# Kernel tuning notes

Measured on AMD Instinct MI355X. Metric: run time of the kernel, lower is better.

The kernel has to match this reference:

```python
import jax, jax.numpy as jnp
import numpy as np

B, N, C, KV = 4, 4096, 1024, 1024
H = 4            # hardcoded 4-way split in the source
Ch, Kh = C // H, KV // H
EPS = 1e-5       # InstanceNorm2d default eps


def setup_inputs() -> dict:
    key = jax.random.key(0)
    ks = jax.random.split(key, 12)
    s = 0.02
    return {
        "emb1":     jax.random.normal(ks[0], (B, N, C),  jnp.float32),
        "emb_all":  jax.random.normal(ks[1], (B, N, KV), jnp.float32),
        "embd1":    jax.random.normal(ks[2], (B, N, C),  jnp.float32),
        "emb_alld": jax.random.normal(ks[3], (B, N, KV), jnp.float32),
        # per-head query weights (distinct per split), torch Linear layout [out,in]
        "Wq":   jax.random.normal(ks[4],  (H, Ch, Ch), jnp.float32) * s,
        "Wqd":  jax.random.normal(ks[5],  (H, Ch, Ch), jnp.float32) * s,
        # source reuses key[0]/value[0] for all splits -> single shared weight
        "Wk0":  jax.random.normal(ks[6],  (Kh, Kh), jnp.float32) * s,
        "Wv0":  jax.random.normal(ks[7],  (Kh, Kh), jnp.float32) * s,
        "Wkd0": jax.random.normal(ks[8],  (Kh, Kh), jnp.float32) * s,
        "Wvd0": jax.random.normal(ks[9],  (Kh, Kh), jnp.float32) * s,
        "Wout":  jax.random.normal(ks[10], (C, C), jnp.float32) * s,
        "Woutd": jax.random.normal(ks[11], (C, C), jnp.float32) * s,
    }


def _inorm(s):
    # InstanceNorm2d(affine=False): normalize over the (C/4, KV/4) plane per (b, head)
    m = s.mean(axis=(2, 3), keepdims=True)
    v = ((s - m) ** 2).mean(axis=(2, 3), keepdims=True)
    return (s - m) * jax.lax.rsqrt(v + EPS)


def reference(emb1, emb_all, embd1, emb_alld,
              Wq, Wqd, Wk0, Wv0, Wkd0, Wvd0, Wout, Woutd):
    scale = 1.0 / np.sqrt(KV).astype(np.float32)
    # split into 4 channel groups and project (Q: per-group weight; K/V: shared weight)
    Q  = jnp.einsum('bnhc,hoc->bhno', emb1.reshape(B, N, H, Ch),  Wq)    # [B,H,N,Ch]
    Qd = jnp.einsum('bnhc,hoc->bhno', embd1.reshape(B, N, H, Ch), Wqd)
    K  = jnp.einsum('bnhk,ok->bhno', emb_all.reshape(B, N, H, Kh),  Wk0)  # [B,H,N,Kh]
    V  = jnp.einsum('bnhk,ok->bhno', emb_all.reshape(B, N, H, Kh),  Wv0)
    Kd = jnp.einsum('bnhk,ok->bhno', emb_alld.reshape(B, N, H, Kh), Wkd0)
    Vd = jnp.einsum('bnhk,ok->bhno', emb_alld.reshape(B, N, H, Kh), Wvd0)
    # channel-attention scores: contract over tokens N -> [B,H,Ch,Kh]
    s1  = jnp.einsum('bhnc,bhnk->bhck', Q,  Kd) * scale
    sd1 = jnp.einsum('bhnc,bhnk->bhck', Qd, K)  * scale
    p1  = jax.nn.softmax(_inorm(s1),  axis=-1)
    pd1 = jax.nn.softmax(_inorm(sd1), axis=-1)
    # context: probs @ V^T -> [b,h,c,n]; permute(0,3,2,1)+view -> [B,N,C] (c-major, h-minor)
    ctx1  = jnp.einsum('bhck,bhnk->bnch', p1,  Vd).reshape(B, N, C)
    ctxd1 = jnp.einsum('bhck,bhnk->bnch', pd1, V ).reshape(B, N, C)
    O1  = ctx1  @ Wout.T
    Od1 = ctxd1 @ Woutd.T
    return (O1, Od1)
```

## Files before the change

kernel.cpp:

```cpp
#include <hip/hip_runtime.h>
#include <math.h>


#define PITCH 40

typedef __bf16 bf16x4 __attribute__((ext_vector_type(4)));
typedef __bf16 bf16x8 __attribute__((ext_vector_type(8)));
typedef float f32x4 __attribute__((ext_vector_type(4)));

__device__ inline void gl2lds16(const void* g, void* l) {
    __builtin_amdgcn_global_load_lds(
        (const __attribute__((address_space(1))) unsigned int*)g,
        (__attribute__((address_space(3))) unsigned int*)l, 16, 0, 0);
}

__global__ __launch_bounds__(256) void prep_x(const float* __restrict__ emb_all,
                                              const float* __restrict__ emb_alld,
                                              __bf16* __restrict__ Xb) {
    const float* src = blockIdx.y ? emb_alld : emb_all;
    __bf16* dst = Xb + (long long)blockIdx.y * 16777216;
    long long i4 = (long long)blockIdx.x * 256 + threadIdx.x;
    float4 v = *(const float4*)&src[i4 * 4];
    bf16x4 o = {(__bf16)v.x, (__bf16)v.y, (__bf16)v.z, (__bf16)v.w};
    *(bf16x4*)&dst[i4 * 4] = o;
}

__global__ __launch_bounds__(256) void prep_w(
    const float* __restrict__ Wq, const float* __restrict__ Wqd,
    const float* __restrict__ Wk0, const float* __restrict__ Wv0,
    const float* __restrict__ Wkd0, const float* __restrict__ Wvd0,
    const float* __restrict__ Wout, const float* __restrict__ Woutd,
    __bf16* __restrict__ Wq_bf, __bf16* __restrict__ Wk_bf,
    __bf16* __restrict__ WvT_bf, __bf16* __restrict__ WoutR_bf)
{
    int id = blockIdx.x * 256 + threadIdx.x;
    if (id < 524288) {
        Wq_bf[id] = (__bf16)(id < 262144 ? Wq[id] : Wqd[id - 262144]);
    } else if (id < 655360) {
        int j = id - 524288;
        Wk_bf[j] = (__bf16)(j < 65536 ? Wkd0[j] : Wk0[j - 65536]);
    } else if (id < 786432) {
        int j = id - 655360;
        int p = j >> 16, r = (j >> 8) & 255, c2 = j & 255;
        const float* s = p ? Wv0 : Wvd0;
        WvT_bf[j] = (__bf16)s[c2 * 256 + r];
    } else if (id < 2883584) {
        int j = id - 786432;
        int p = j >> 20; int rem = j & 1048575; int h = rem >> 18; int oc = rem & 262143;
        int o = oc >> 8, c = oc & 255;
        const float* s = p ? Woutd : Wout;
        WoutR_bf[j] = (__bf16)s[o * 1024 + c * 4 + h];
    }
}

__global__ __launch_bounds__(256) void gram_mfma(
    const float* __restrict__ emb1, const float* __restrict__ emb_all,
    const float* __restrict__ embd1, const float* __restrict__ emb_alld,
    float* __restrict__ Gpart)
{
    __shared__ __bf16 As[128 * PITCH];
    __shared__ __bf16 Bs[128 * PITCH];

    const int z = blockIdx.z;
    const int path = z >> 4, bh = z & 15;
    const int b = bh >> 2, h = bh & 3;
    const float* Xm = (path == 0 ? emb_alld : emb_all) + (long long)b * 4194304 + h * 256;
    const float* Xn = (path == 0 ? emb1     : embd1)   + (long long)b * 4194304 + h * 256;

    const int i0 = (blockIdx.x >> 1) * 128;
    const int j0 = (blockIdx.x & 1) * 128;
    const int kb0 = blockIdx.y * 1024;

    const int t = threadIdx.x;
    const int q  = t & 7;
    const int i4 = t >> 3;
    const int lane = t & 63;
    const int wave = t >> 6;
    const int wr = (wave >> 1) * 64, wc = (wave & 1) * 64;
    const int fm = lane & 15, fg = lane >> 4;

    f32x4 acc[4][4];
#pragma unroll
    for (int u = 0; u < 4; ++u)
#pragma unroll
        for (int v = 0; v < 4; ++v) acc[u][v] = (f32x4){0.f, 0.f, 0.f, 0.f};

    for (int kb = kb0; kb < kb0 + 1024; kb += 32) {
        float4 va[4], vb[4];
        const float* pa = Xm + (long long)(kb + q * 4) * 1024 + i0 + i4 * 4;
        const float* pb = Xn + (long long)(kb + q * 4) * 1024 + j0 + i4 * 4;
#pragma unroll
        for (int r = 0; r < 4; ++r) {
            va[r] = *(const float4*)(pa + (long long)r * 1024);
            vb[r] = *(const float4*)(pb + (long long)r * 1024);
        }
        __syncthreads();
#pragma unroll
        for (int c = 0; c < 4; ++c) {
            bf16x4 wa, wb;
#pragma unroll
            for (int r = 0; r < 4; ++r) {
                wa[r] = (__bf16)(((const float*)&va[r])[c]);
                wb[r] = (__bf16)(((const float*)&vb[r])[c]);
            }
            *(bf16x4*)&As[(i4 * 4 + c) * PITCH + q * 4] = wa;
            *(bf16x4*)&Bs[(i4 * 4 + c) * PITCH + q * 4] = wb;
        }
        __syncthreads();

        bf16x8 af[4], bfv[4];
#pragma unroll
        for (int mt = 0; mt < 4; ++mt)
            af[mt] = *(const bf16x8*)&As[(wr + mt * 16 + fm) * PITCH + fg * 8];
#pragma unroll
        for (int nt = 0; nt < 4; ++nt)
            bfv[nt] = *(const bf16x8*)&Bs[(wc + nt * 16 + fm) * PITCH + fg * 8];
#pragma unroll
        for (int mt = 0; mt < 4; ++mt)
#pragma unroll
            for (int nt = 0; nt < 4; ++nt)
                acc[mt][nt] = __builtin_amdgcn_mfma_f32_16x16x32_bf16(af[mt], bfv[nt], acc[mt][nt], 0, 0, 0);
    }

    float* Gp = Gpart + ((long long)blockIdx.y * 32 + z) * 65536;
    const int col = lane & 15, rq = (lane >> 4) * 4;
#pragma unroll
    for (int mt = 0; mt < 4; ++mt)
#pragma unroll
        for (int nt = 0; nt < 4; ++nt)
#pragma unroll
            for (int r = 0; r < 4; ++r)
                Gp[(i0 + wr + mt * 16 + rq + r) * 256 + (j0 + wc + nt * 16 + col)] = acc[mt][nt][r];
}

__global__ __launch_bounds__(256) void reduce_g(const float* __restrict__ Gpart, __bf16* __restrict__ GT) {
    long long idx4 = (long long)blockIdx.x * 256 + threadIdx.x;
    float4 a = *(const float4*)&Gpart[idx4 * 4];
    float4 b = *(const float4*)&Gpart[2097152 + idx4 * 4];
    float4 c = *(const float4*)&Gpart[4194304 + idx4 * 4];
    float4 d = *(const float4*)&Gpart[6291456 + idx4 * 4];
    bf16x4 o;
    o[0] = (__bf16)(a.x + b.x + c.x + d.x);
    o[1] = (__bf16)(a.y + b.y + c.y + d.y);
    o[2] = (__bf16)(a.z + b.z + c.z + d.z);
    o[3] = (__bf16)(a.w + b.w + c.w + d.w);
    *(bf16x4*)&GT[idx4 * 4] = o;
}

template <typename CT>
__global__ __launch_bounds__(256) void mfma_nt(
    const __bf16* __restrict__ A, const __bf16* __restrict__ B, CT* __restrict__ C,
    int mtiles, int K,
    long long a1, long long a2, long long a3,
    long long b1, long long b2, long long b3,
    long long c1, long long c2, long long c3,
    int cpitch, float alpha)
{
    __shared__ __bf16 As[64 * 32];
    __shared__ __bf16 Bs[64 * 32];
    const int z = blockIdx.y;
    const __bf16* Az = A + (long long)(z >> 4) * a1 + (long long)((z >> 2) & 3) * a2 + (long long)(z & 3) * a3;
    const __bf16* Bz = B + (long long)(z >> 4) * b1 + (long long)((z >> 2) & 3) * b2 + (long long)(z & 3) * b3;
    CT* Cz = C + (long long)(z >> 4) * c1 + (long long)((z >> 2) & 3) * c2 + (long long)(z & 3) * c3;

    const int tm = blockIdx.x % mtiles, tn = blockIdx.x / mtiles;
    const int t = threadIdx.x;
    const int lane = t & 63, wave = t >> 6;
    const int row = t >> 2, ch = t & 3;
    const int fm = lane & 15, fg = lane >> 4;

    const __bf16* ga = Az + (long long)(tm * 64 + row) * K + ch * 8;
    const __bf16* gb = Bz + (long long)(tn * 64 + row) * K + ch * 8;
    __bf16* la = &As[t * 8];
    __bf16* lb = &Bs[t * 8];

    f32x4 acc[4];
#pragma unroll
    for (int u = 0; u < 4; ++u) acc[u] = (f32x4){0.f, 0.f, 0.f, 0.f};

    for (int kb = 0; kb < K; kb += 32) {
        __syncthreads();
        gl2lds16(ga + kb, la);
        gl2lds16(gb + kb, lb);
        __syncthreads();
        bf16x8 bv = *(const bf16x8*)&Bs[(wave * 16 + fm) * 32 + fg * 8];
#pragma unroll
        for (int mt = 0; mt < 4; ++mt) {
            bf16x8 av = *(const bf16x8*)&As[(mt * 16 + fm) * 32 + fg * 8];
            acc[mt] = __builtin_amdgcn_mfma_f32_16x16x32_bf16(av, bv, acc[mt], 0, 0, 0);
        }
    }

    const int colc = tn * 64 + wave * 16 + fm;
    const int rq = fg * 4;
#pragma unroll
    for (int mt = 0; mt < 4; ++mt)
#pragma unroll
        for (int r = 0; r < 4; ++r) {
            int rowc = tm * 64 + mt * 16 + rq + r;
            Cz[(long long)rowc * cpitch + colc] = (CT)(acc[mt][r] * alpha);
        }
}

__global__ __launch_bounds__(256) void obig_mfma(
    const __bf16* __restrict__ Xall, const __bf16* __restrict__ Mb, float* __restrict__ out)
{
    __shared__ __bf16 As[128 * 32];
    __shared__ __bf16 Bs[128 * 32];

    const int z = blockIdx.z;
    const int path = z >> 2, b = z & 3;
    const __bf16* X = Xall + (path == 0 ? 16777216LL : 0LL) + (long long)b * 4194304;
    const __bf16* Bm = Mb + (long long)path * 4194304 + (long long)b * 1048576;
    float* Ob = out + (long long)path * 16777216 + (long long)b * 4194304;

    const int m0 = blockIdx.x * 128;
    const int o0 = blockIdx.y * 128;

    const int t = threadIdx.x;
    const int lane = t & 63, wave = t >> 6;
    const int wr = (wave >> 1) * 64, wc = (wave & 1) * 64;
    const int fm = lane & 15, fg = lane >> 4;
    const int row = t >> 2, ch = t & 3;

    const __bf16* ga0 = X + (long long)(m0 + row) * 1024 + ch * 8;
    const __bf16* ga1 = X + (long long)(m0 + 64 + row) * 1024 + ch * 8;
    const __bf16* gb0 = Bm + (long long)(o0 + row) * 1024 + ch * 8;
    const __bf16* gb1 = Bm + (long long)(o0 + 64 + row) * 1024 + ch * 8;
    __bf16* la0 = &As[t * 8];
    __bf16* la1 = &As[2048 + t * 8];
    __bf16* lb0 = &Bs[t * 8];
    __bf16* lb1 = &Bs[2048 + t * 8];

    f32x4 acc[4][4];
#pragma unroll
    for (int u = 0; u < 4; ++u)
#pragma unroll
        for (int v = 0; v < 4; ++v) acc[u][v] = (f32x4){0.f, 0.f, 0.f, 0.f};

    for (int kb = 0; kb < 1024; kb += 32) {
        __syncthreads();
        gl2lds16(ga0 + kb, la0);
        gl2lds16(ga1 + kb, la1);
        gl2lds16(gb0 + kb, lb0);
        gl2lds16(gb1 + kb, lb1);
        __syncthreads();

        bf16x8 af[4], bv[4];
#pragma unroll
        for (int mt = 0; mt < 4; ++mt)
            af[mt] = *(const bf16x8*)&As[(wr + mt * 16 + fm) * 32 + fg * 8];
#pragma unroll
        for (int nt = 0; nt < 4; ++nt)
            bv[nt] = *(const bf16x8*)&Bs[(wc + nt * 16 + fm) * 32 + fg * 8];
#pragma unroll
        for (int mt = 0; mt < 4; ++mt)
#pragma unroll
            for (int nt = 0; nt < 4; ++nt)
                acc[mt][nt] = __builtin_amdgcn_mfma_f32_16x16x32_bf16(af[mt], bv[nt], acc[mt][nt], 0, 0, 0);
    }

    const int col = lane & 15, rq = (lane >> 4) * 4;
#pragma unroll
    for (int mt = 0; mt < 4; ++mt)
#pragma unroll
        for (int nt = 0; nt < 4; ++nt)
#pragma unroll
            for (int r = 0; r < 4; ++r)
                Ob[(long long)(m0 + wr + mt * 16 + rq + r) * 1024 + (o0 + wc + nt * 16 + col)] = acc[mt][nt][r];
}

__global__ __launch_bounds__(256) void stats_kernel(const float* __restrict__ S, float* __restrict__ st) {
    int pg = blockIdx.x;
    const float* s = S + (long long)pg * 65536;
    float sum = 0.f, sq = 0.f;
    for (int i = threadIdx.x; i < 65536; i += 256) {
        float v = s[i];
        sum += v;
        sq += v * v;
    }
#pragma unroll
    for (int off = 32; off; off >>= 1) {
        sum += __shfl_down(sum, off);
        sq  += __shfl_down(sq,  off);
    }
    __shared__ float r1[4], r2[4];
    int w = threadIdx.x >> 6;
    if ((threadIdx.x & 63) == 0) { r1[w] = sum; r2[w] = sq; }
    __syncthreads();
    if (threadIdx.x == 0) {
        float ts = r1[0] + r1[1] + r1[2] + r1[3];
        float tq = r2[0] + r2[1] + r2[2] + r2[3];
        float mean = ts * (1.0f / 65536.0f);
        float var = tq * (1.0f / 65536.0f) - mean * mean;
        st[pg * 2 + 0] = mean;
        st[pg * 2 + 1] = rsqrtf(var + 1e-5f);
    }
}

__global__ __launch_bounds__(256) void softmax_kernel(const float* __restrict__ S,
                                                      const float* __restrict__ st,
                                                      __bf16* __restrict__ p_bf) {
    int pg = blockIdx.y;
    int c = blockIdx.x;
    float mean = st[pg * 2 + 0], rstd = st[pg * 2 + 1];
    const float* row = S + (long long)pg * 65536 + c * 256;
    int t = threadIdx.x;
    float x = (row[t] - mean) * rstd;
    float m = x;
#pragma unroll
    for (int off = 32; off; off >>= 1) m = fmaxf(m, __shfl_down(m, off));
    __shared__ float r1[4], r2[4];
    int w = t >> 6;
    if ((t & 63) == 0) r1[w] = m;
    __syncthreads();
    m = fmaxf(fmaxf(r1[0], r1[1]), fmaxf(r1[2], r1[3]));
    float e = expf(x - m);
    float ssum = e;
#pragma unroll
    for (int off = 32; off; off >>= 1) ssum += __shfl_down(ssum, off);
    if ((t & 63) == 0) r2[w] = ssum;
    __syncthreads();
    ssum = r2[0] + r2[1] + r2[2] + r2[3];
    p_bf[(long long)pg * 65536 + c * 256 + t] = (__bf16)(e / ssum);
}

extern "C" void kernel_launch(void* const* d_in, const int* in_sizes, int n_in,
                              void* d_out, int out_size, void* d_ws, size_t ws_size,
                              hipStream_t stream) {
    const float* emb1     = (const float*)d_in[0];
    const float* emb_all  = (const float*)d_in[1];
    const float* embd1    = (const float*)d_in[2];
    const float* emb_alld = (const float*)d_in[3];
    const float* Wq    = (const float*)d_in[4];
    const float* Wqd   = (const float*)d_in[5];
    const float* Wk0   = (const float*)d_in[6];
    const float* Wv0   = (const float*)d_in[7];
    const float* Wkd0  = (const float*)d_in[8];
    const float* Wvd0  = (const float*)d_in[9];
    const float* Wout  = (const float*)d_in[10];
    const float* Woutd = (const float*)d_in[11];
    float* out = (float*)d_out;

    float* ws = (float*)d_ws;
    float*  Gpart   = ws;
    __bf16* Mb_bf   = (__bf16*)ws;
    __bf16* X_bf    = (__bf16*)(ws + 8388608);
    __bf16* GT_bf   = (__bf16*)(ws + 25165824);
    __bf16* T_bf    = (__bf16*)(ws + 26214400);
    float*  S       = ws + 27262976;
    __bf16* p_bf    = (__bf16*)(ws + 29360128);
    __bf16* PT_bf   = (__bf16*)(ws + 30408704);
    __bf16* Wq_bf   = (__bf16*)(ws + 31457280);
    __bf16* Wk_bf   = (__bf16*)(ws + 31719424);
    __bf16* WvT_bf  = (__bf16*)(ws + 31784960);
    __bf16* WoutR_bf= (__bf16*)(ws + 31850496);
    float*  st      = ws + 32899072;

    dim3 blk(256);

    prep_x<<<dim3(16384, 2), blk, 0, stream>>>(emb_all, emb_alld, X_bf);
    prep_w<<<11264, blk, 0, stream>>>(Wq, Wqd, Wk0, Wv0, Wkd0, Wvd0, Wout, Woutd,
                                      Wq_bf, Wk_bf, WvT_bf, WoutR_bf);

    gram_mfma<<<dim3(4, 4, 32), blk, 0, stream>>>(emb1, emb_all, embd1, emb_alld, Gpart);
    reduce_g<<<2048, blk, 0, stream>>>(Gpart, GT_bf);

    mfma_nt<__bf16><<<dim3(16, 32), blk, 0, stream>>>(
        Wq_bf, GT_bf, T_bf, 4, 256,
        262144, 0, 65536,  1048576, 262144, 65536,  1048576, 262144, 65536, 256, 1.0f);
    mfma_nt<float><<<dim3(16, 32), blk, 0, stream>>>(
        T_bf, Wk_bf, S, 4, 256,
        1048576, 262144, 65536,  65536, 0, 0,  1048576, 262144, 65536, 256, 0.03125f);

    stats_kernel<<<32, blk, 0, stream>>>(S, st);
    softmax_kernel<<<dim3(256, 32), blk, 0, stream>>>(S, st, p_bf);

    mfma_nt<__bf16><<<dim3(16, 32), blk, 0, stream>>>(
        WvT_bf, p_bf, PT_bf, 4, 256,
        65536, 0, 0,  1048576, 262144, 65536,  1048576, 262144, 65536, 256, 1.0f);
    mfma_nt<__bf16><<<dim3(64, 32), blk, 0, stream>>>(
        WoutR_bf, PT_bf, Mb_bf, 16, 256,
        1048576, 0, 262144,  1048576, 262144, 65536,  4194304, 1048576, 256, 1024, 1.0f);

    obig_mfma<<<dim3(32, 8, 8), blk, 0, stream>>>(X_bf, Mb_bf, out);
}
```

Before: 623.6 us.

## Rewrite final output GEMM as 256x256 tiled, double-buffered, swizzled 8-wave kernel

Replaces the 128x128 single-buffered output GEMM with a 256x256-tile kernel using 512 threads and 64-wide K steps. Loads go straight from global memory into LDS, split into half-tile stages that are double-buffered and hidden behind MFMA quadrants using manual vmcnt waits and barriers. LDS columns are XOR-swizzled to avoid bank conflicts, and the block IDs are remapped so neighbouring blocks share L2 data. The aim is to raise MFMA utilisation and cut global and LDS traffic, at the cost of a 128KB LDS footprint, heavy register use and delicate hand-written synchronisation.

```diff
diff --git a/kernel.cpp b/kernel.cpp
--- a/kernel.cpp
+++ b/kernel.cpp
@@ -202,72 +202,158 @@
         }
 }
 
-__global__ __launch_bounds__(256) void obig_mfma(
+
+#define VMCNT4 asm volatile("s_waitcnt vmcnt(4)" ::: "memory")
+#define VMCNT2 asm volatile("s_waitcnt vmcnt(2)" ::: "memory")
+#define VMCNT0 asm volatile("s_waitcnt vmcnt(0)" ::: "memory")
+#define BARR   asm volatile("s_barrier" ::: "memory")
+
+#define STAGE_A(h, kt, c) do { \
+    _Pragma("unroll") \
+    for (int o = 0; o < 2; ++o) { \
+        int rl = (h) * 64 + o * 128 + stg_row; \
+        gl2lds16(Xa + (long long)rl * 1024 + (kt) * 64 + stg_col, \
+                 &lds[(c) * 32768 + rl * 64 + lin_col]); \
+    } \
+} while (0)
+
+#define STAGE_B(h, kt, c) do { \
+    _Pragma("unroll") \
+    for (int o = 0; o < 2; ++o) { \
+        int rl = o * 128 + (h) * 32 + (stg_row & 31) + ((stg_row & 32) << 1); \
+        gl2lds16(Bb + (long long)rl * 1024 + (kt) * 64 + stg_col, \
+                 &lds[(c) * 32768 + 16384 + rl * 64 + lin_col]); \
+    } \
+} while (0)
+
+#define LOAD_A(hm, c) do { \
+    _Pragma("unroll") \
+    for (int mt = 0; mt < 4; ++mt) { \
+        const __bf16* p = &lds[(c) * 32768 + (wr * 128 + (hm) * 64 + mt * 16 + fm) * 64]; \
+        af[mt][0] = *(const bf16x8*)&p[(fg * 8) ^ rsw]; \
+        af[mt][1] = *(const bf16x8*)&p[(32 + fg * 8) ^ rsw]; \
+    } \
+} while (0)
+
+#define LOAD_B(hn, c) do { \
+    _Pragma("unroll") \
+    for (int nt = 0; nt < 2; ++nt) { \
+        const __bf16* p = &lds[(c) * 32768 + 16384 + (wc * 64 + (hn) * 32 + nt * 16 + fm) * 64]; \
+        bv[(hn) * 2 + nt][0] = *(const bf16x8*)&p[(fg * 8) ^ rsw]; \
+        bv[(hn) * 2 + nt][1] = *(const bf16x8*)&p[(32 + fg * 8) ^ rsw]; \
+    } \
+} while (0)
+
+#define MFMA_Q(hm, hn) do { \
+    __builtin_amdgcn_s_setprio(1); \
+    _Pragma("unroll") \
+    for (int mt = 0; mt < 4; ++mt) \
+        _Pragma("unroll") \
+        for (int nt = 0; nt < 2; ++nt) { \
+            acc[(hm) * 4 + mt][(hn) * 2 + nt] = __builtin_amdgcn_mfma_f32_16x16x32_bf16( \
+                af[mt][0], bv[(hn) * 2 + nt][0], acc[(hm) * 4 + mt][(hn) * 2 + nt], 0, 0, 0); \
+            acc[(hm) * 4 + mt][(hn) * 2 + nt] = __builtin_amdgcn_mfma_f32_16x16x32_bf16( \
+                af[mt][1], bv[(hn) * 2 + nt][1], acc[(hm) * 4 + mt][(hn) * 2 + nt], 0, 0, 0); \
+        } \
+    __builtin_amdgcn_s_setprio(0); \
+} while (0)
+
+__global__ __launch_bounds__(512, 2) void obig8(
     const __bf16* __restrict__ Xall, const __bf16* __restrict__ Mb, float* __restrict__ out)
 {
-    __shared__ __bf16 As[128 * 32];
-    __shared__ __bf16 Bs[128 * 32];
-
-    const int z = blockIdx.z;
+    __shared__ __bf16 lds[65536];
+
+    const int id = blockIdx.x;
+    const int wg = (id & 7) * 64 + (id >> 3);
+    const int z = wg >> 6;
+    const int tile = wg & 63;
+    const int tm = tile & 15, tn = tile >> 4;
     const int path = z >> 2, b = z & 3;
-    const __bf16* X = Xall + (path == 0 ? 16777216LL : 0LL) + (long long)b * 4194304;
-    const __bf16* Bm = Mb + (long long)path * 4194304 + (long long)b * 1048576;
+
+    const __bf16* Xa = Xall + (path == 0 ? 16777216LL : 0LL)
+                     + (long long)b * 4194304 + (long long)tm * 262144;
+    const __bf16* Bb = Mb + (long long)path * 4194304 + (long long)b * 1048576
+                     + (long long)tn * 262144;
     float* Ob = out + (long long)path * 16777216 + (long long)b * 4194304;
-
-    const int m0 = blockIdx.x * 128;
-    const int o0 = blockIdx.y * 128;
 
     const int t = threadIdx.x;
     const int lane = t & 63, wave = t >> 6;
-    const int wr = (wave >> 1) * 64, wc = (wave & 1) * 64;
+    const int wr = wave >> 2, wc = wave & 3;
     const int fm = lane & 15, fg = lane >> 4;
-    const int row = t >> 2, ch = t & 3;
-
-    const __bf16* ga0 = X + (long long)(m0 + row) * 1024 + ch * 8;
-    const __bf16* ga1 = X + (long long)(m0 + 64 + row) * 1024 + ch * 8;
-    const __bf16* gb0 = Bm + (long long)(o0 + row) * 1024 + ch * 8;
-    const __bf16* gb1 = Bm + (long long)(o0 + 64 + row) * 1024 + ch * 8;
-    __bf16* la0 = &As[t * 8];
-    __bf16* la1 = &As[2048 + t * 8];
-    __bf16* lb0 = &Bs[t * 8];
-    __bf16* lb1 = &Bs[2048 + t * 8];
-
-    f32x4 acc[4][4];
-#pragma unroll
-    for (int u = 0; u < 4; ++u)
+    const int stg_row = t >> 3;
+    const int lin_col = (t & 7) * 8;
+    const int stg_col = ((t & 7) ^ (stg_row & 7)) * 8;
+    const int rsw = (fm & 7) * 8;
+
+    f32x4 acc[8][4];
+#pragma unroll
+    for (int u = 0; u < 8; ++u)
 #pragma unroll
         for (int v = 0; v < 4; ++v) acc[u][v] = (f32x4){0.f, 0.f, 0.f, 0.f};
 
-    for (int kb = 0; kb < 1024; kb += 32) {
-        __syncthreads();
-        gl2lds16(ga0 + kb, la0);
-        gl2lds16(ga1 + kb, la1);
-        gl2lds16(gb0 + kb, lb0);
-        gl2lds16(gb1 + kb, lb1);
-        __syncthreads();
-
-        bf16x8 af[4], bv[4];
-#pragma unroll
-        for (int mt = 0; mt < 4; ++mt)
-            af[mt] = *(const bf16x8*)&As[(wr + mt * 16 + fm) * 32 + fg * 8];
-#pragma unroll
-        for (int nt = 0; nt < 4; ++nt)
-            bv[nt] = *(const bf16x8*)&Bs[(wc + nt * 16 + fm) * 32 + fg * 8];
-#pragma unroll
-        for (int mt = 0; mt < 4; ++mt)
-#pragma unroll
-            for (int nt = 0; nt < 4; ++nt)
-                acc[mt][nt] = __builtin_amdgcn_mfma_f32_16x16x32_bf16(af[mt], bv[nt], acc[mt][nt], 0, 0, 0);
-    }
-
-    const int col = lane & 15, rq = (lane >> 4) * 4;
-#pragma unroll
-    for (int mt = 0; mt < 4; ++mt)
-#pragma unroll
-        for (int nt = 0; nt < 4; ++nt)
+    bf16x8 af[4][2];
+    bf16x8 bv[8][2];
+
+    STAGE_A(0, 0, 0);
+    STAGE_B(0, 0, 0);
+    STAGE_B(1, 0, 0);
+    STAGE_A(1, 0, 0);
+    VMCNT4;
+    BARR;
+
+    for (int kt = 0; kt < 15; ++kt) {
+        const int c = kt & 1, n = c ^ 1;
+        LOAD_A(0, c);
+        LOAD_B(0, c);
+        STAGE_A(0, kt + 1, n);
+        VMCNT4;
+        BARR;
+        MFMA_Q(0, 0);
+        BARR;
+        LOAD_B(1, c);
+        STAGE_B(0, kt + 1, n);
+        VMCNT4;
+        BARR;
+        MFMA_Q(0, 1);
+        BARR;
+        LOAD_A(1, c);
+        STAGE_B(1, kt + 1, n);
+        BARR;
+        MFMA_Q(1, 1);
+        BARR;
+        STAGE_A(1, kt + 1, n);
+        VMCNT4;
+        BARR;
+        MFMA_Q(1, 0);
+        BARR;
+    }
+
+    {
+        LOAD_A(0, 1);
+        LOAD_B(0, 1);
+        VMCNT2;
+        BARR;
+        MFMA_Q(0, 0);
+        BARR;
+        LOAD_B(1, 1);
+        VMCNT0;
+        BARR;
+        MFMA_Q(0, 1);
+        BARR;
+        LOAD_A(1, 1);
+        MFMA_Q(1, 1);
+        MFMA_Q(1, 0);
+    }
+
+    const int rq = fg * 4;
+    float* op = Ob + (long long)(tm * 256 + wr * 128 + rq) * 1024 + tn * 256 + wc * 64 + fm;
+#pragma unroll
+    for (int mi = 0; mi < 8; ++mi)
+#pragma unroll
+        for (int ni = 0; ni < 4; ++ni)
 #pragma unroll
             for (int r = 0; r < 4; ++r)
-                Ob[(long long)(m0 + wr + mt * 16 + rq + r) * 1024 + (o0 + wc + nt * 16 + col)] = acc[mt][nt][r];
+                op[(long long)(mi * 16 + r) * 1024 + ni * 16] = acc[mi][ni][r];
 }
 
 __global__ __launch_bounds__(256) void stats_kernel(const float* __restrict__ S, float* __restrict__ st) {
@@ -383,5 +469,5 @@
         WoutR_bf, PT_bf, Mb_bf, 16, 256,
         1048576, 0, 262144,  1048576, 262144, 65536,  4194304, 1048576, 256, 1024, 1.0f);
 
-    obig_mfma<<<dim3(32, 8, 8), blk, 0, stream>>>(X_bf, Mb_bf, out);
-}
+    obig8<<<dim3(512), dim3(512), 0, stream>>>(X_bf, Mb_bf, out);
+}
```

Measured after the change: 568.9 us. 8.8% less time.
